# Optimization experiments

Hardware: AMD Instinct MI355X
Metric: run time of the kernel (lower is better)

Reference implementation:

```python
import jax, jax.numpy as jnp
import numpy as np

# Faithful math of the torch module (dropout in eval mode => identity):
#   alpha = sigmoid(smoothing_weight)                       # [h,1] -> [1,1,h,1]
#   out[t] = alpha^(t+1) * v0 + sum_{s<=t} (1-alpha) alpha^(t-s) * values[s]
#   aux path kernel: weight/clamp(1-alpha,1e-6)*alpha => factor*alpha^(t-s+1)
#     with factor = (1-alpha)/max(1-alpha,1e-6) (== 1 unless alpha ~ 1)
# The torch code realizes this causal linear recurrence via FFT cross-correlation;
# here we use an associative (parallel) scan, which computes the same sums.

B, T, H, D = 8, 4096, 8, 64

def setup_inputs() -> dict:
    key = jax.random.key(0)
    k1, k2, k3, k4 = jax.random.split(key, 4)
    values = jax.random.normal(k1, (B, T, H, D), dtype=jnp.float32)
    aux_values = jax.random.normal(k2, (B, T, H, D), dtype=jnp.float32)
    v0 = jax.random.normal(k3, (1, 1, H, D), dtype=jnp.float32)
    smoothing_weight = jax.random.normal(k4, (H, 1), dtype=jnp.float32)
    return {"values": values, "aux_values": aux_values, "v0": v0,
            "smoothing_weight": smoothing_weight}

def reference(values, aux_values, v0, smoothing_weight):
    b, t, h, d = values.shape
    alpha = jax.nn.sigmoid(smoothing_weight).reshape(1, 1, h, 1)  # [1,1,h,1]
    one_m = 1.0 - alpha
    factor = one_m / jnp.maximum(one_m, 1e-6)  # == 1 unless alpha ~ 1 (clamp in torch)
    # Linear recurrence y[t] = alpha*y[t-1] + u[t], y[-1] = v0, where
    # u[t] = (1-alpha)*values[t] + factor*alpha*aux_values[t] (fused main + aux path).
    a = jnp.broadcast_to(alpha, (1, t, h, 1))               # decay coeffs
    u = one_m * values + (factor * alpha) * aux_values      # [b,t,h,d]
    def combine(c1, c2):
        a1, b1 = c1
        a2, b2 = c2
        return (a1 * a2, a2 * b1 + b2)
    A, Bsum = jax.lax.associative_scan(combine, (a, u), axis=1)
    # A[t] = alpha^(t+1); Bsum[t] = sum_{s<=t} alpha^(t-s) * u[s]
    return A * v0 + Bsum
```

## Files before the change

### kernel.cpp

```cpp
#include <hip/hip_runtime.h>
#include <math.h>

#define BB 8
#define TT 4096
#define HH 8
#define DD 64
#define NC 128
#define LL (TT / NC)

__device__ __forceinline__ float sigmoidf_(float x) {
    return 1.0f / (1.0f + expf(-x));
}

__global__ __launch_bounds__(128)
void k_partial(const float4* __restrict__ vals, const float4* __restrict__ aux,
               const float* __restrict__ w, float4* __restrict__ Z) {
    const int blk = blockIdx.x;
    const int b = blk / NC, c = blk % NC;
    const int tid = threadIdx.x;
    const int h = tid >> 4;
    const int d4 = tid & 15;

    const float alpha = sigmoidf_(w[h]);
    const float onem  = 1.0f - alpha;
    const float fa    = (onem / fmaxf(onem, 1e-6f)) * alpha;

    const int t0 = c * LL;
    int base = (b * TT + t0) * 128 + h * 16 + d4;

    float4 y = make_float4(0.f, 0.f, 0.f, 0.f);
#pragma unroll 8
    for (int i = 0; i < LL; ++i) {
        float4 v = vals[base + i * 128];
        float4 a = aux[base + i * 128];
        y.x = alpha * y.x + (onem * v.x + fa * a.x);
        y.y = alpha * y.y + (onem * v.y + fa * a.y);
        y.z = alpha * y.z + (onem * v.z + fa * a.z);
        y.w = alpha * y.w + (onem * v.w + fa * a.w);
    }
    Z[(b * NC + c) * 128 + tid] = y;
}

__global__ __launch_bounds__(256)
void k_scan(const float* __restrict__ Z, const float* __restrict__ v0,
            const float* __restrict__ w, float* __restrict__ P) {
    const int g = blockIdx.x * 256 + threadIdx.x;
    const int b = g >> 9;
    const int r = g & 511;
    const int h = r >> 6;

    const float alpha = sigmoidf_(w[h]);
    const float aL = powf(alpha, (float)LL);

    float p = v0[r];
    P[(b * NC + 0) * 512 + r] = p;
    for (int c = 1; c < NC; ++c) {
        p = aL * p + Z[(b * NC + (c - 1)) * 512 + r];
        P[(b * NC + c) * 512 + r] = p;
    }
}

__global__ __launch_bounds__(128)
void k_final(const float4* __restrict__ vals, const float4* __restrict__ aux,
             const float* __restrict__ w, const float4* __restrict__ P,
             float4* __restrict__ out) {
    const int blk = blockIdx.x;
    const int b = blk / NC, c = blk % NC;
    const int tid = threadIdx.x;
    const int h = tid >> 4;
    const int d4 = tid & 15;

    const float alpha = sigmoidf_(w[h]);
    const float onem  = 1.0f - alpha;
    const float fa    = (onem / fmaxf(onem, 1e-6f)) * alpha;

    const int t0 = c * LL;
    int base = (b * TT + t0) * 128 + h * 16 + d4;

    float4 y = P[(b * NC + c) * 128 + tid];
#pragma unroll 8
    for (int i = 0; i < LL; ++i) {
        float4 v = vals[base + i * 128];
        float4 a = aux[base + i * 128];
        y.x = alpha * y.x + (onem * v.x + fa * a.x);
        y.y = alpha * y.y + (onem * v.y + fa * a.y);
        y.z = alpha * y.z + (onem * v.z + fa * a.z);
        y.w = alpha * y.w + (onem * v.w + fa * a.w);
        out[base + i * 128] = y;
    }
}

extern "C" void kernel_launch(void* const* d_in, const int* in_sizes, int n_in,
                              void* d_out, int out_size, void* d_ws, size_t ws_size,
                              hipStream_t stream) {
    const float4* vals = (const float4*)d_in[0];
    const float4* aux  = (const float4*)d_in[1];
    const float*  v0   = (const float*)d_in[2];
    const float*  w    = (const float*)d_in[3];
    float4* out = (float4*)d_out;

    float* Z = (float*)d_ws;
    float* P = Z + (size_t)BB * NC * 512;

    k_partial<<<BB * NC, 128, 0, stream>>>(vals, aux, w, (float4*)Z);
    k_scan<<<(BB * HH * DD) / 256, 256, 0, stream>>>(Z, v0, w, P);
    k_final<<<BB * NC, 128, 0, stream>>>(vals, aux, w, (const float4*)P, out);
}
```

Baseline: 209.2 us.

## Write local scan in first pass, parallelize chunk scan, add carry correction

Result: faster. 196.5 us (-6.1%).

```diff
diff --git a/kernel.cpp b/kernel.cpp
--- a/kernel.cpp
+++ b/kernel.cpp
@@ -5,7 +5,7 @@
 #define TT 4096
 #define HH 8
 #define DD 64
-#define NC 128
+#define NC 256
 #define LL (TT / NC)
 
 __device__ __forceinline__ float sigmoidf_(float x) {
@@ -14,71 +14,21 @@
 
 __global__ __launch_bounds__(128)
 void k_partial(const float4* __restrict__ vals, const float4* __restrict__ aux,
-               const float* __restrict__ w, float4* __restrict__ Z) {
+               const float* __restrict__ w, float4* __restrict__ out,
+               float4* __restrict__ Z) {
     const int blk = blockIdx.x;
     const int b = blk / NC, c = blk % NC;
     const int tid = threadIdx.x;
     const int h = tid >> 4;
-    const int d4 = tid & 15;
 
     const float alpha = sigmoidf_(w[h]);
     const float onem  = 1.0f - alpha;
     const float fa    = (onem / fmaxf(onem, 1e-6f)) * alpha;
 
-    const int t0 = c * LL;
-    int base = (b * TT + t0) * 128 + h * 16 + d4;
+    int base = (b * TT + c * LL) * 128 + tid;
 
     float4 y = make_float4(0.f, 0.f, 0.f, 0.f);
-#pragma unroll 8
-    for (int i = 0; i < LL; ++i) {
-        float4 v = vals[base + i * 128];
-        float4 a = aux[base + i * 128];
-        y.x = alpha * y.x + (onem * v.x + fa * a.x);
-        y.y = alpha * y.y + (onem * v.y + fa * a.y);
-        y.z = alpha * y.z + (onem * v.z + fa * a.z);
-        y.w = alpha * y.w + (onem * v.w + fa * a.w);
-    }
-    Z[(b * NC + c) * 128 + tid] = y;
-}
-
-__global__ __launch_bounds__(256)
-void k_scan(const float* __restrict__ Z, const float* __restrict__ v0,
-            const float* __restrict__ w, float* __restrict__ P) {
-    const int g = blockIdx.x * 256 + threadIdx.x;
-    const int b = g >> 9;
-    const int r = g & 511;
-    const int h = r >> 6;
-
-    const float alpha = sigmoidf_(w[h]);
-    const float aL = powf(alpha, (float)LL);
-
-    float p = v0[r];
-    P[(b * NC + 0) * 512 + r] = p;
-    for (int c = 1; c < NC; ++c) {
-        p = aL * p + Z[(b * NC + (c - 1)) * 512 + r];
-        P[(b * NC + c) * 512 + r] = p;
-    }
-}
-
-__global__ __launch_bounds__(128)
-void k_final(const float4* __restrict__ vals, const float4* __restrict__ aux,
-             const float* __restrict__ w, const float4* __restrict__ P,
-             float4* __restrict__ out) {
-    const int blk = blockIdx.x;
-    const int b = blk / NC, c = blk % NC;
-    const int tid = threadIdx.x;
-    const int h = tid >> 4;
-    const int d4 = tid & 15;
-
-    const float alpha = sigmoidf_(w[h]);
-    const float onem  = 1.0f - alpha;
-    const float fa    = (onem / fmaxf(onem, 1e-6f)) * alpha;
-
-    const int t0 = c * LL;
-    int base = (b * TT + t0) * 128 + h * 16 + d4;
-
-    float4 y = P[(b * NC + c) * 128 + tid];
-#pragma unroll 8
+#pragma unroll
     for (int i = 0; i < LL; ++i) {
         float4 v = vals[base + i * 128];
         float4 a = aux[base + i * 128];
@@ -87,6 +37,99 @@
         y.z = alpha * y.z + (onem * v.z + fa * a.z);
         y.w = alpha * y.w + (onem * v.w + fa * a.w);
         out[base + i * 128] = y;
+    }
+    Z[(b * NC + c) * 128 + tid] = y;
+}
+
+__global__ __launch_bounds__(256)
+void k_scan(const float4* __restrict__ Z, const float* __restrict__ v0,
+            const float* __restrict__ w, float4* __restrict__ P) {
+    __shared__ float lds[NC][33];
+
+    const int blk = blockIdx.x;
+    const int b  = blk >> 4;
+    const int h  = (blk >> 1) & 7;
+    const int dh = blk & 1;
+    const int r4base = h * 16 + dh * 8;
+    const int tid = threadIdx.x;
+
+    const float alpha = sigmoidf_(w[h]);
+    const float aL = powf(alpha, (float)LL);
+
+#pragma unroll
+    for (int it = 0; it < 8; ++it) {
+        int idx = it * 256 + tid;
+        int c = idx >> 3, k = idx & 7;
+        float4 z = Z[(b * NC + c) * 128 + r4base + k];
+        lds[c][k * 4 + 0] = z.x;
+        lds[c][k * 4 + 1] = z.y;
+        lds[c][k * 4 + 2] = z.z;
+        lds[c][k * 4 + 3] = z.w;
+    }
+    __syncthreads();
+
+    const int c = tid;
+    float s[32];
+#pragma unroll
+    for (int k = 0; k < 32; ++k) s[k] = lds[c][k];
+
+    float m = aL;
+    for (int off = 1; off < NC; off <<= 1) {
+        float tmp[32];
+        const bool act = (c >= off);
+        if (act) {
+#pragma unroll
+            for (int k = 0; k < 32; ++k) tmp[k] = lds[c - off][k];
+        }
+        __syncthreads();
+        if (act) {
+#pragma unroll
+            for (int k = 0; k < 32; ++k) { s[k] += m * tmp[k]; lds[c][k] = s[k]; }
+        }
+        m *= m;
+        __syncthreads();
+    }
+
+    const float pc = powf(alpha, (float)(LL * c));
+    const float4* v04 = (const float4*)v0;
+#pragma unroll
+    for (int k = 0; k < 8; ++k) {
+        float4 vv = v04[r4base + k];
+        float4 pr;
+        if (c == 0) {
+            pr = vv;
+        } else {
+            pr.x = pc * vv.x + lds[c - 1][k * 4 + 0];
+            pr.y = pc * vv.y + lds[c - 1][k * 4 + 1];
+            pr.z = pc * vv.z + lds[c - 1][k * 4 + 2];
+            pr.w = pc * vv.w + lds[c - 1][k * 4 + 3];
+        }
+        P[(b * NC + c) * 128 + r4base + k] = pr;
+    }
+}
+
+__global__ __launch_bounds__(128)
+void k_final(const float* __restrict__ w, const float4* __restrict__ P,
+             float4* __restrict__ out) {
+    const int blk = blockIdx.x;
+    const int b = blk / NC, c = blk % NC;
+    const int tid = threadIdx.x;
+    const int h = tid >> 4;
+
+    const float alpha = sigmoidf_(w[h]);
+    const float4 p = P[(b * NC + c) * 128 + tid];
+    int base = (b * TT + c * LL) * 128 + tid;
+
+    float coef = alpha;
+#pragma unroll
+    for (int i = 0; i < LL; ++i) {
+        float4 o = out[base + i * 128];
+        o.x += coef * p.x;
+        o.y += coef * p.y;
+        o.z += coef * p.z;
+        o.w += coef * p.w;
+        out[base + i * 128] = o;
+        coef *= alpha;
     }
 }
 
@@ -99,10 +142,10 @@
     const float*  w    = (const float*)d_in[3];
     float4* out = (float4*)d_out;
 
-    float* Z = (float*)d_ws;
-    float* P = Z + (size_t)BB * NC * 512;
+    float4* Z = (float4*)d_ws;
+    float4* P = Z + (size_t)BB * NC * 128;
 
-    k_partial<<<BB * NC, 128, 0, stream>>>(vals, aux, w, (float4*)Z);
-    k_scan<<<(BB * HH * DD) / 256, 256, 0, stream>>>(Z, v0, w, P);
-    k_final<<<BB * NC, 128, 0, stream>>>(vals, aux, w, (const float4*)P, out);
+    k_partial<<<BB * NC, 128, 0, stream>>>(vals, aux, w, out, Z);
+    k_scan<<<BB * HH * 2, 256, 0, stream>>>(Z, v0, w, P);
+    k_final<<<BB * NC, 128, 0, stream>>>(w, P, out);
 }
```
